# Optimization experiments

Hardware: AMD Instinct MI355X
Metric: run time of the kernel (lower is better)

The kernel has to match this reference:

```python
import jax, jax.numpy as jnp
import numpy as np

D_MODEL = 256
KSIZE = 16
EPS = 1e-5


def conv1d(x, w, b):
    # x: [B, C, N], w: [O, C, K], SAME padding over node axis
    y = jax.lax.conv_general_dilated(x, w, window_strides=(1,), padding='SAME',
                                     dimension_numbers=('NCH', 'OIH', 'NCH'))
    return y + b[None, :, None]


def layernorm(x, g, b):
    mu = jnp.mean(x, axis=-1, keepdims=True)
    var = jnp.mean(jnp.square(x - mu), axis=-1, keepdims=True)
    return (x - mu) * jax.lax.rsqrt(var + EPS) * g + b


def setup_inputs() -> dict:
    key = jax.random.key(0)
    ks = jax.random.split(key, 16)
    B, N, d, K = 4, 2048, D_MODEL, KSIZE
    conv_scale = 1.0 / np.sqrt(d * K)
    lin_scale = 1.0 / np.sqrt(d)
    return {
        'src': jax.random.normal(ks[0], (B, N, d), jnp.float32),
        'x_lst': jnp.zeros((B, N, N), jnp.float32),
        'adj': jax.random.randint(ks[1], (B, N, N), 0, 2, jnp.int32),
        'dis': jax.random.uniform(ks[2], (B, N, N), jnp.float32),
        'Wq': jax.random.normal(ks[3], (d, d, K), jnp.float32) * conv_scale,
        'bq': jnp.zeros((d,), jnp.float32),
        'Wk': jax.random.normal(ks[4], (d, d, K), jnp.float32) * conv_scale,
        'bk': jnp.zeros((d,), jnp.float32),
        'Wv': jax.random.normal(ks[5], (d, d, K), jnp.float32) * conv_scale,
        'bv': jnp.zeros((d,), jnp.float32),
        'W1': jax.random.normal(ks[6], (d, d), jnp.float32) * lin_scale,
        'b1': jnp.zeros((d,), jnp.float32),
        'W2': jax.random.normal(ks[7], (d, d), jnp.float32) * lin_scale,
        'b2': jnp.zeros((d,), jnp.float32),
        'W3': jax.random.normal(ks[8], (d, d), jnp.float32) * lin_scale,
        'b3': jnp.zeros((d,), jnp.float32),
        'g1': jnp.ones((d,), jnp.float32),
        'be1': jnp.zeros((d,), jnp.float32),
        'g2': jnp.ones((d,), jnp.float32),
        'be2': jnp.zeros((d,), jnp.float32),
    }


def reference(src, x_lst, adj, dis, Wq, bq, Wk, bk, Wv, bv,
              W1, b1, W2, b2, W3, b3, g1, be1, g2, be2):
    # ---- _ga_block: transpose to channel-major, graph attention ----
    x = jnp.swapaxes(src, -2, -1)                      # [B, d, N]
    q = conv1d(x, Wq, bq)                              # [B, d, N]
    k = conv1d(x, Wk, bk)
    v = conv1d(x, Wv, bv)
    scale = 1.0 / jnp.sqrt(jnp.asarray(D_MODEL, src.dtype))
    scores = jnp.einsum('bdn,bdm->bnm', q, k) * scale  # [B, N, N]
    scores = scores - dis                              # distance bias
    scores = jnp.where(adj > 0, scores, jnp.asarray(-1e9, scores.dtype))
    attn = jax.nn.softmax(scores, axis=-1)             # [B, N, N]
    x_lst_new = x_lst + attn                           # accumulated attention state
    out = jnp.einsum('bnm,bdm->bdn', attn, v)          # [B, d, N]
    x1 = jnp.swapaxes(out, -2, -1)                     # [B, N, d] (dropout = identity in eval)
    # ---- residual + norm1 ----
    h = layernorm(src + x1, g1, be1)
    # ---- 3-layer LeakyReLU MLP + residual + norm2 ----
    m = jax.nn.leaky_relu(h @ W1.T + b1)
    m = jax.nn.leaky_relu(m @ W2.T + b2)
    m = m @ W3.T + b3
    h = layernorm(h + m, g2, be2)
    return h, x_lst_new
```

## Files before the change

kernel.cpp:

```cpp
#include <hip/hip_runtime.h>
#include <stdint.h>

typedef _Float16 h16;
typedef _Float16 h4v __attribute__((ext_vector_type(4)));
typedef _Float16 h8v __attribute__((ext_vector_type(8)));
typedef float    f4v __attribute__((ext_vector_type(4)));
typedef int      i4v __attribute__((ext_vector_type(4)));

#define NBATCH 4
#define NNODE  2048
#define DM     256
#define NPAD   2063
#define QKELEM 2097152
#define PARTN  (8192 * 256)

__device__ __forceinline__ void async16(const void* g, void* l) {
#if __has_builtin(__builtin_amdgcn_global_load_lds)
  __builtin_amdgcn_global_load_lds((__attribute__((address_space(1))) void*)g,
                                   (__attribute__((address_space(3))) void*)l, 16, 0, 0);
#else
  *(f4v*)l = *(const f4v*)g;
#endif
}

#define BARRIER() do { asm volatile("" ::: "memory"); __builtin_amdgcn_s_barrier(); asm volatile("" ::: "memory"); } while (0)
#define MFMA16 __builtin_amdgcn_mfma_f32_16x16x32_f16

__device__ __forceinline__ void gemm_tile(
    const h16* Abase, int astride,
    const h16* Bbase, int bstride,
    h16* As, h16* Bs, f4v acc[4][4], int kiters)
{
  const int tid  = threadIdx.x;
  const int lane = tid & 63;
  const int wv   = tid >> 6;
  const int srow = tid >> 2;
  const int sch  = ((tid & 3) ^ ((tid >> 3) & 3)) * 8;
  const h16* gA0 = Abase + (long)srow * astride + sch;
  const h16* gA1 = Abase + (long)(srow + 64) * astride + sch;
  const h16* gB0 = Bbase + (long)srow * bstride + sch;
  const h16* gB1 = Bbase + (long)(srow + 64) * bstride + sch;
  h16* lA0 = As + tid * 8;
  h16* lA1 = As + 2048 + tid * 8;
  h16* lB0 = Bs + tid * 8;
  h16* lB1 = Bs + 2048 + tid * 8;
  const int swz = ((lane & 15) >> 1) & 3;
  const int qq  = ((lane >> 4) ^ swz) * 8;
  const int amr = ((wv & 1) * 64 + (lane & 15)) * 32 + qq;
  const int bnr = ((wv >> 1) * 64 + (lane & 15)) * 32 + qq;

  for (int kt = 0; kt < kiters; ++kt) {
    const int k0 = kt * 32;
    __syncthreads();
    async16(gA0 + k0, lA0);
    async16(gA1 + k0, lA1);
    async16(gB0 + k0, lB0);
    async16(gB1 + k0, lB1);
    asm volatile("s_waitcnt vmcnt(0)" ::: "memory");
    __syncthreads();
    h8v af[4], bf[4];
#pragma unroll
    for (int i = 0; i < 4; ++i) af[i] = *(const h8v*)(As + amr + i * 512);
#pragma unroll
    for (int j = 0; j < 4; ++j) bf[j] = *(const h8v*)(Bs + bnr + j * 512);
#pragma unroll
    for (int i = 0; i < 4; ++i)
#pragma unroll
      for (int j = 0; j < 4; ++j)
        acc[i][j] = MFMA16(af[i], bf[j], acc[i][j], 0, 0, 0);
  }
}

__device__ __forceinline__ void zero_acc(f4v acc[4][4]) {
#pragma unroll
  for (int i = 0; i < 4; ++i)
#pragma unroll
    for (int j = 0; j < 4; ++j) {
      f4v z = {0.f, 0.f, 0.f, 0.f};
      acc[i][j] = z;
    }
}

template<int ASTRIDE, int BSTRIDE>
__device__ __forceinline__ void gemm256_pipe(
    const h16* __restrict__ Abase, const h16* __restrict__ Bbase,
    h16* As, h16* Bs, f4v (&acc)[8][4], const int kiters)
{
  const int tid  = threadIdx.x;
  const int lane = tid & 63, wv = tid >> 6;

  const int rh = tid >> 3;
  const int cs = (((tid & 7) ^ ((tid >> 3) & 7)) << 3);
  const h16* AgT = Abase + (long)rh * ASTRIDE + cs;
  const h16* BgT = Bbase + (long)rh * BSTRIDE + cs;
  h16* lA = As + tid * 8;
  h16* lB = Bs + tid * 8;

  auto stageA = [&](int kt, int half) {
    h16* d = lA + ((kt & 1) << 14) + (half << 13);
    const h16* g = AgT + (long)half * 128 * ASTRIDE + kt * 64;
    async16(g, d);
    async16(g + 64 * ASTRIDE, d + 4096);
  };
  auto stageB = [&](int kt, int half) {
    h16* d = lB + ((kt & 1) << 14) + (half << 13);
    const h16* g = BgT + (long)half * 128 * BSTRIDE + kt * 64;
    async16(g, d);
    async16(g + 64 * BSTRIDE, d + 4096);
  };

  const int wr = wv >> 2, wc = wv & 3;
  const int e0 = (((lane >> 4) ^ (lane & 7)) << 3);
  const int e1 = e0 ^ 32;
  const h16* pA0 = As + (wr * 128 + (lane & 15)) * 64 + e0;
  const h16* pA1 = pA0 + (e1 - e0);
  const h16* pB0 = Bs + (wc * 64 + (lane & 15)) * 64 + e0;
  const h16* pB1 = pB0 + (e1 - e0);

#pragma unroll
  for (int i = 0; i < 8; ++i)
#pragma unroll
    for (int j = 0; j < 4; ++j) { f4v z = {0.f, 0.f, 0.f, 0.f}; acc[i][j] = z; }

  stageA(0, 0); stageA(0, 1); stageB(0, 0); stageB(0, 1); stageA(1, 0);
  asm volatile("s_waitcnt vmcnt(2)" ::: "memory");
  BARRIER();

#pragma unroll 1
  for (int kt = 0; kt < kiters; ++kt) {
    const int sb = (kt & 1) << 14;
    h8v ar[4][2], bL[2][2], bR[2][2];
#pragma unroll
    for (int i = 0; i < 4; ++i) {
      ar[i][0] = *(const h8v*)(pA0 + sb + i * 1024);
      ar[i][1] = *(const h8v*)(pA1 + sb + i * 1024);
    }
#pragma unroll
    for (int j = 0; j < 2; ++j) {
      bL[j][0] = *(const h8v*)(pB0 + sb + j * 1024);
      bL[j][1] = *(const h8v*)(pB1 + sb + j * 1024);
    }
    if (kt < kiters - 1) stageA(kt + 1, 1);
    BARRIER();
    __builtin_amdgcn_s_setprio(1);
#pragma unroll
    for (int i = 0; i < 4; ++i)
#pragma unroll
      for (int j = 0; j < 2; ++j) {
        acc[i][j] = MFMA16(ar[i][0], bL[j][0], acc[i][j], 0, 0, 0);
        acc[i][j] = MFMA16(ar[i][1], bL[j][1], acc[i][j], 0, 0, 0);
      }
    __builtin_amdgcn_s_setprio(0);
    BARRIER();
#pragma unroll
    for (int j = 0; j < 2; ++j) {
      bR[j][0] = *(const h8v*)(pB0 + sb + (j + 2) * 1024);
      bR[j][1] = *(const h8v*)(pB1 + sb + (j + 2) * 1024);
    }
    if (kt < kiters - 1) stageB(kt + 1, 0);
    BARRIER();
    __builtin_amdgcn_s_setprio(1);
#pragma unroll
    for (int i = 0; i < 4; ++i)
#pragma unroll
      for (int j = 0; j < 2; ++j) {
        acc[i][j + 2] = MFMA16(ar[i][0], bR[j][0], acc[i][j + 2], 0, 0, 0);
        acc[i][j + 2] = MFMA16(ar[i][1], bR[j][1], acc[i][j + 2], 0, 0, 0);
      }
    __builtin_amdgcn_s_setprio(0);
    BARRIER();
#pragma unroll
    for (int i = 0; i < 4; ++i) {
      ar[i][0] = *(const h8v*)(pA0 + sb + (i + 4) * 1024);
      ar[i][1] = *(const h8v*)(pA1 + sb + (i + 4) * 1024);
    }
    if (kt < kiters - 1) stageB(kt + 1, 1);
    BARRIER();
    __builtin_amdgcn_s_setprio(1);
#pragma unroll
    for (int i = 0; i < 4; ++i)
#pragma unroll
      for (int j = 0; j < 2; ++j) {
        acc[i + 4][j + 2] = MFMA16(ar[i][0], bR[j][0], acc[i + 4][j + 2], 0, 0, 0);
        acc[i + 4][j + 2] = MFMA16(ar[i][1], bR[j][1], acc[i + 4][j + 2], 0, 0, 0);
      }
    __builtin_amdgcn_s_setprio(0);
    BARRIER();
#pragma unroll
    for (int j = 0; j < 2; ++j) {
      bL[j][0] = *(const h8v*)(pB0 + sb + j * 1024);
      bL[j][1] = *(const h8v*)(pB1 + sb + j * 1024);
    }
    if (kt < kiters - 2) {
      stageA(kt + 2, 0);
      asm volatile("s_waitcnt vmcnt(2)" ::: "memory");
    } else if (kt == kiters - 2) {
      asm volatile("s_waitcnt vmcnt(0)" ::: "memory");
    }
    BARRIER();
    __builtin_amdgcn_s_setprio(1);
#pragma unroll
    for (int i = 0; i < 4; ++i)
#pragma unroll
      for (int j = 0; j < 2; ++j) {
        acc[i + 4][j] = MFMA16(ar[i][0], bL[j][0], acc[i + 4][j], 0, 0, 0);
        acc[i + 4][j] = MFMA16(ar[i][1], bL[j][1], acc[i + 4][j], 0, 0, 0);
      }
    __builtin_amdgcn_s_setprio(0);
    BARRIER();
  }
}

#define NSRC_BLK 8252
__global__ __launch_bounds__(256) void prep_all_kernel(
    const float* __restrict__ src,
    const float* __restrict__ Wq, const float* __restrict__ Wk, const float* __restrict__ Wv,
    const float* __restrict__ W1, const float* __restrict__ W2, const float* __restrict__ W3,
    h16* __restrict__ Xpad, h16* __restrict__ Wt, h16* __restrict__ Wl)
{
  __shared__ float plds[16][257];
  const int bi = blockIdx.x, tid = threadIdx.x;
  if (bi < NSRC_BLK) {
    int idx = bi * 256 + tid;
    int c = idx & 255;
    int row = idx >> 8;
    int b = row / NPAD;
    int n = row - b * NPAD;
    float v = 0.f;
    int ns = n - 7;
    if (ns >= 0 && ns < NNODE) v = src[((long)b * NNODE + ns) * DM + c];
    Xpad[idx] = (h16)v;
  } else if (bi < NSRC_BLK + 768) {
    const int q = bi - NSRC_BLK;
    const int w = q >> 8, o = q & 255;
    const float* W = (w == 0) ? Wq : (w == 1) ? Wk : Wv;
    const float* base = W + (long)o * 4096;
    f4v r0 = *(const f4v*)(base + tid * 16);
    f4v r1 = *(const f4v*)(base + tid * 16 + 4);
    f4v r2 = *(const f4v*)(base + tid * 16 + 8);
    f4v r3 = *(const f4v*)(base + tid * 16 + 12);
#pragma unroll
    for (int k = 0; k < 4; ++k) {
      plds[k][tid] = r0[k]; plds[4 + k][tid] = r1[k];
      plds[8 + k][tid] = r2[k]; plds[12 + k][tid] = r3[k];
    }
    __syncthreads();
    const int t = tid >> 4, c0 = (tid & 15) * 16;
    h16* out = Wt + ((long)(w * 256 + o)) * 4096 + t * 256 + c0;
    h8v o0, o1;
#pragma unroll
    for (int k = 0; k < 8; ++k) { o0[k] = (h16)plds[t][c0 + k]; o1[k] = (h16)plds[t][c0 + 8 + k]; }
    *(h8v*)out = o0;
    *(h8v*)(out + 8) = o1;
  } else {
    int idx = (bi - NSRC_BLK - 768) * 256 + tid;
    int w = idx >> 16;
    int rem = idx & 65535;
    const float* W = (w == 0) ? W1 : (w == 1) ? W2 : W3;
    Wl[idx] = (h16)W[rem];
  }
}

__global__ __launch_bounds__(512) void conv_gemm256_kernel(
    const h16* __restrict__ Xpad, const h16* __restrict__ Wt,
    h16* __restrict__ Qp, h16* __restrict__ Kp, h16* __restrict__ Vp)
{
  __shared__ __align__(16) h16 As[32768];
  __shared__ __align__(16) h16 Bs[32768];
  const int lane = threadIdx.x & 63, wv = threadIdx.x >> 6;
  const int mt = blockIdx.x, w = blockIdx.y, ks = blockIdx.z;
  const int m0 = mt * 256;
  const int b  = m0 >> 11, n0 = m0 & 2047;

  const h16* Abase = Xpad + ((long)(b * NPAD + n0) << 8) + ((long)ks << 11);
  const h16* Bbase = Wt + ((long)w << 20) + ((long)ks << 11);

  f4v acc[8][4];
  gemm256_pipe<256, 4096>(Abase, Bbase, As, Bs, acc, 32);

  h16* dst = ((w == 0) ? Qp : (w == 1) ? Kp : Vp) + (long)ks * QKELEM;
  const int wr = wv >> 2, wc = wv & 3;
  const int rb = (lane >> 4) * 4;
  const int cb = wc * 64 + (lane & 15);
  const int mrow0 = m0 + wr * 128;
#pragma unroll
  for (int i = 0; i < 8; ++i)
#pragma unroll
    for (int j = 0; j < 4; ++j) {
      const int gc = cb + j * 16;
#pragma unroll
      for (int e = 0; e < 4; ++e) {
        const int gr = mrow0 + i * 16 + rb + e;
        dst[(long)gr * 256 + gc] = (h16)acc[i][j][e];
      }
    }
}

__global__ __launch_bounds__(256) void conv_reduce_kernel(
    const h16* __restrict__ Qp, const h16* __restrict__ Kp, const h16* __restrict__ Vp,
    const float* __restrict__ bq, const float* __restrict__ bk, const float* __restrict__ bv,
    h16* __restrict__ Qb, h16* __restrict__ Kb, h16* __restrict__ Vt)
{
  __shared__ float T[64][65];
  const int bi = blockIdx.x, tid = threadIdx.x;
  if (bi < 2048) {
    const long gid = (long)bi * 256 + tid;
    const int which = gid >= (QKELEM / 8);
    const long e = (gid - (long)which * (QKELEM / 8)) * 8;
    const h16* P = which ? Kp : Qp;
    const float* bias = which ? bk : bq;
    h8v p0 = *(const h8v*)(P + e);
    h8v p1 = *(const h8v*)(P + QKELEM + e);
    const int c0 = (int)(e & 255);
    h8v o;
#pragma unroll
    for (int k = 0; k < 8; ++k) o[k] = (h16)((float)p0[k] + (float)p1[k] + bias[c0 + k]);
    *(h8v*)((which ? Kb : Qb) + e) = o;
  } else {
    const int q = bi - 2048;
    const int mt = q >> 2, ct = q & 3;
    const int m0 = mt * 64, c0 = ct * 64;
    const int b = m0 >> 11, n0 = m0 & 2047;
    const int rr = tid >> 3, cc = (tid & 7) * 8;
#pragma unroll
    for (int p = 0; p < 2; ++p) {
      const int r = p * 32 + rr;
      const long so = (long)(m0 + r) * 256 + c0 + cc;
      h8v p0 = *(const h8v*)(Vp + so);
      h8v p1 = *(const h8v*)(Vp + QKELEM + so);
#pragma unroll
      for (int e = 0; e < 8; ++e) T[r][cc + e] = (float)p0[e] + (float)p1[e];
    }
    __syncthreads();
#pragma unroll
    for (int p = 0; p < 2; ++p) {
      const int d = p * 32 + rr;
      const float bias_v = bv[c0 + d];
      h8v o;
#pragma unroll
      for (int e = 0; e < 8; ++e) o[e] = (h16)(T[cc + e][d] + bias_v);
      *(h8v*)(Vt + ((long)(b * 256 + c0 + d)) * 2048 + n0 + cc) = o;
    }
  }
}

__global__ __launch_bounds__(512) void scores_gemm256_kernel(
    const h16* __restrict__ Q, const h16* __restrict__ Km, h16* __restrict__ Sh)
{
  __shared__ __align__(16) h16 As[32768];
  __shared__ __align__(16) h16 Bs[32768];
  const int lane = threadIdx.x & 63, wv = threadIdx.x >> 6;
  const int nt = blockIdx.x, mt = blockIdx.y, b = blockIdx.z;

  const h16* Abase = Q + ((long)b * NNODE + nt * 256) * 256;
  const h16* Bbase = Km + ((long)b * NNODE + mt * 256) * 256;

  f4v acc[8][4];
  gemm256_pipe<256, 256>(Abase, Bbase, As, Bs, acc, 4);

  const int wr = wv >> 2, wc = wv & 3;
  const int rb = (lane >> 4) * 4;
  const int cb = wc * 64 + (lane & 15);
  h16* Srow = Sh + (long)b * NNODE * NNODE;
  const int row0 = nt * 256 + wr * 128;
  const int col0 = mt * 256;
#pragma unroll
  for (int i = 0; i < 8; ++i) {
#pragma unroll
    for (int e = 0; e < 4; ++e) {
      const long row = row0 + i * 16 + rb + e;
#pragma unroll
      for (int j = 0; j < 4; ++j) {
        const int col = col0 + cb + j * 16;
        Srow[row * 2048 + col] = (h16)(acc[i][j][e] * 0.0625f);
      }
    }
  }
}

__global__ __launch_bounds__(256) void softmax_kernel(
    h16* __restrict__ Sh, const float* __restrict__ dis, const int* __restrict__ adj,
    const float* __restrict__ x_lst, float* __restrict__ out_x)
{
  const int r = blockIdx.x;
  const long ro = (long)r * 2048;
  const int tid = threadIdx.x, lane = tid & 63, wv = tid >> 6;
  const int j0 = tid * 4;
  __shared__ float wmax[4], wsum[4];

  h4v sv0 = *(const h4v*)(Sh + ro + j0);
  h4v sv1 = *(const h4v*)(Sh + ro + 1024 + j0);
  f4v d0 = *(const f4v*)(dis + ro + j0);
  f4v d1 = *(const f4v*)(dis + ro + 1024 + j0);
  i4v a0 = *(const i4v*)(adj + ro + j0);
  i4v a1 = *(const i4v*)(adj + ro + 1024 + j0);

  float s[8];
#pragma unroll
  for (int k = 0; k < 4; ++k) s[k]     = (a0[k] > 0) ? ((float)sv0[k] - d0[k]) : -1e9f;
#pragma unroll
  for (int k = 0; k < 4; ++k) s[k + 4] = (a1[k] > 0) ? ((float)sv1[k] - d1[k]) : -1e9f;

  float m = s[0];
#pragma unroll
  for (int k = 1; k < 8; ++k) m = fmaxf(m, s[k]);
#pragma unroll
  for (int off = 32; off > 0; off >>= 1) m = fmaxf(m, __shfl_xor(m, off, 64));
  if (lane == 0) wmax[wv] = m;
  __syncthreads();
  m = fmaxf(fmaxf(wmax[0], wmax[1]), fmaxf(wmax[2], wmax[3]));

  float p[8], ls = 0.f;
#pragma unroll
  for (int k = 0; k < 8; ++k) { p[k] = __expf(s[k] - m); ls += p[k]; }
#pragma unroll
  for (int off = 32; off > 0; off >>= 1) ls += __shfl_xor(ls, off, 64);
  if (lane == 0) wsum[wv] = ls;
  __syncthreads();
  const float inv = 1.0f / (wsum[0] + wsum[1] + wsum[2] + wsum[3]);

  f4v x0 = *(const f4v*)(x_lst + ro + j0);
  f4v x1 = *(const f4v*)(x_lst + ro + 1024 + j0);
  f4v o0, o1;
  h4v pv0, pv1;
#pragma unroll
  for (int k = 0; k < 4; ++k) {
    const float a = p[k] * inv, bq = p[k + 4] * inv;
    o0[k] = x0[k] + a; o1[k] = x1[k] + bq;
    pv0[k] = (h16)a; pv1[k] = (h16)bq;
  }
  *(f4v*)(out_x + ro + j0) = o0;
  *(f4v*)(out_x + ro + 1024 + j0) = o1;
  *(h4v*)(Sh + ro + j0) = pv0;
  *(h4v*)(Sh + ro + 1024 + j0) = pv1;
}

__global__ __launch_bounds__(256) void av_gemm_kernel(
    const h16* __restrict__ Attn, const h16* __restrict__ Vt, h16* __restrict__ X1p)
{
  __shared__ __align__(16) h16 As[4096];
  __shared__ __align__(16) h16 Bs[4096];
  const int nt = blockIdx.x, b = blockIdx.z;
  const int ct = blockIdx.y & 1, ks = blockIdx.y >> 1;
  const h16* Abase = Attn + ((long)b * NNODE + nt * 128) * 2048 + ks * 1024;
  const h16* Bbase = Vt + ((long)b * 256 + ct * 128) * 2048 + ks * 1024;
  f4v acc[4][4];
  zero_acc(acc);
  gemm_tile(Abase, 2048, Bbase, 2048, As, Bs, acc, 32);

  const int lane = threadIdx.x & 63, wv = threadIdx.x >> 6;
  const int rbase = (wv & 1) * 64 + (lane >> 4) * 4;
  const int cbase = (wv >> 1) * 64 + (lane & 15);
  h16* dst = X1p + (long)ks * PARTN;
#pragma unroll
  for (int i = 0; i < 4; ++i) {
#pragma unroll
    for (int e = 0; e < 4; ++e) {
      const long row = (long)b * NNODE + nt * 128 + rbase + i * 16 + e;
#pragma unroll
      for (int j = 0; j < 4; ++j) {
        const int col = ct * 128 + cbase + j * 16;
        dst[row * 256 + col] = (h16)acc[i][j][e];
      }
    }
  }
}

__device__ __forceinline__ float wred_sum(float v) {
#pragma unroll
  for (int off = 32; off > 0; off >>= 1) v += __shfl_xor(v, off, 64);
  return v;
}

__global__ __launch_bounds__(256) void ln1_kernel(
    const float* __restrict__ X, const h16* __restrict__ Y, const h16* __restrict__ Y2,
    const float* __restrict__ g, const float* __restrict__ bb,
    float* __restrict__ outF, h16* __restrict__ outH)
{
  const int wv = threadIdx.x >> 6, lane = threadIdx.x & 63;
  const long r = (long)blockIdx.x * 4 + wv;
  const long off = r * 256 + lane * 4;
  f4v x = *(const f4v*)(X + off);
  h4v y = *(const h4v*)(Y + off);
  h4v y2 = *(const h4v*)(Y2 + off);
  float v[4];
  float sum = 0.f, sq = 0.f;
#pragma unroll
  for (int k = 0; k < 4; ++k) {
    v[k] = x[k] + (float)y[k] + (float)y2[k];
    sum += v[k]; sq += v[k] * v[k];
  }
  sum = wred_sum(sum);
  sq  = wred_sum(sq);
  const float mu = sum * (1.0f / 256.0f);
  const float var = sq * (1.0f / 256.0f) - mu * mu;
  const float rs = rsqrtf(var + 1e-5f);
  f4v gg = *(const f4v*)(g + lane * 4);
  f4v be = *(const f4v*)(bb + lane * 4);
  f4v o;
#pragma unroll
  for (int k = 0; k < 4; ++k) o[k] = (v[k] - mu) * rs * gg[k] + be[k];
  *(f4v*)(outF + off) = o;
  h4v hv;
#pragma unroll
  for (int k = 0; k < 4; ++k) hv[k] = (h16)o[k];
  *(h4v*)(outH + off) = hv;
}

__global__ __launch_bounds__(256) void mlp_fused_kernel(
    const h16* __restrict__ H16, const float* __restrict__ Hf,
    const h16* __restrict__ Wl,
    const float* __restrict__ b1, const float* __restrict__ b2, const float* __restrict__ b3,
    const float* __restrict__ g2, const float* __restrict__ be2,
    float* __restrict__ out_h)
{
  __shared__ h16 Xa[32][264];
  __shared__ h16 Xb[32][264];
  __shared__ __align__(16) h16 Bs[8192];
  const int tid = threadIdx.x, lane = tid & 63, wv = tid >> 6;
  const int m0 = blockIdx.x * 32;

  {
    const int r = tid >> 3, cq = (tid & 7) * 32;
    const h16* s = H16 + (long)(m0 + r) * 256 + cq;
#pragma unroll
    for (int k = 0; k < 4; ++k)
      *(h8v*)&Xa[r][cq + k * 8] = *(const h8v*)(s + k * 8);
  }

  const int srow = tid >> 2;
  const int sch  = ((tid & 3) ^ ((tid >> 3) & 3)) * 8;
  h16* lB = Bs + tid * 8;
  const int quad = lane >> 4;
  const float* biases[3] = {b1, b2, b3};

  for (int layer = 0; layer < 3; ++layer) {
    const h16* W = Wl + layer * 65536;
    const h16 (*Xi)[264] = (layer == 1) ? (const h16(*)[264])Xb : (const h16(*)[264])Xa;
    h16 (*Xo)[264] = (layer == 1) ? Xa : Xb;
    f4v acc[2][4];
#pragma unroll
    for (int i = 0; i < 2; ++i)
#pragma unroll
      for (int j = 0; j < 4; ++j) { f4v z = {0.f,0.f,0.f,0.f}; acc[i][j] = z; }

    for (int kt = 0; kt < 8; ++kt) {
      __syncthreads();
      const h16* gB = W + (long)srow * 256 + kt * 32 + sch;
      async16(gB, lB);
      async16(gB + 64 * 256, lB + 64 * 32);
      async16(gB + 128 * 256, lB + 128 * 32);
      async16(gB + 192 * 256, lB + 192 * 32);
      asm volatile("s_waitcnt vmcnt(0)" ::: "memory");
      __syncthreads();
      h8v af[2], bf[4];
#pragma unroll
      for (int i = 0; i < 2; ++i)
        af[i] = *(const h8v*)&Xi[i * 16 + (lane & 15)][kt * 32 + quad * 8];
#pragma unroll
      for (int j = 0; j < 4; ++j) {
        const int n = wv * 64 + j * 16 + (lane & 15);
        const int q = (quad ^ ((n >> 1) & 3)) * 8;
        bf[j] = *(const h8v*)(Bs + n * 32 + q);
      }
#pragma unroll
      for (int i = 0; i < 2; ++i)
#pragma unroll
        for (int j = 0; j < 4; ++j)
          acc[i][j] = MFMA16(af[i], bf[j], acc[i][j], 0, 0, 0);
    }
    const int rb = quad * 4;
    const int cb = wv * 64 + (lane & 15);
    const float* bias = biases[layer];
    const bool leaky = (layer < 2);
#pragma unroll
    for (int j = 0; j < 4; ++j) {
      const int col = cb + j * 16;
      const float bv = bias[col];
#pragma unroll
      for (int i = 0; i < 2; ++i)
#pragma unroll
        for (int e = 0; e < 4; ++e) {
          float v = acc[i][j][e] + bv;
          if (leaky) v = (v >= 0.f) ? v : 0.01f * v;
          Xo[i * 16 + rb + e][col] = (h16)v;
        }
    }
  }
  __syncthreads();

  const int r = tid >> 3, c0 = (tid & 7) * 32;
  const float* hrow = Hf + (long)(m0 + r) * 256 + c0;
  float v[32];
  float s = 0.f, sq = 0.f;
#pragma unroll
  for (int k8 = 0; k8 < 8; ++k8) {
    f4v h4 = *(const f4v*)(hrow + k8 * 4);
#pragma unroll
    for (int e = 0; e < 4; ++e) {
      float t = (float)Xb[r][c0 + k8 * 4 + e] + h4[e];
      v[k8 * 4 + e] = t; s += t; sq += t * t;
    }
  }
#pragma unroll
  for (int off = 1; off < 8; off <<= 1) { s += __shfl_xor(s, off, 64); sq += __shfl_xor(sq, off, 64); }
  const float mu = s * (1.0f / 256.0f);
  const float var = sq * (1.0f / 256.0f) - mu * mu;
  const float rs = rsqrtf(var + 1e-5f);
  float* orow = out_h + (long)(m0 + r) * 256 + c0;
#pragma unroll
  for (int k8 = 0; k8 < 8; ++k8) {
    f4v gg = *(const f4v*)(g2 + c0 + k8 * 4);
    f4v be = *(const f4v*)(be2 + c0 + k8 * 4);
    f4v o;
#pragma unroll
    for (int e = 0; e < 4; ++e) o[e] = (v[k8 * 4 + e] - mu) * rs * gg[e] + be[e];
    *(f4v*)(orow + k8 * 4) = o;
  }
}

extern "C" void kernel_launch(void* const* d_in, const int* in_sizes, int n_in,
                              void* d_out, int out_size, void* d_ws, size_t ws_size,
                              hipStream_t stream)
{
  const float* src  = (const float*)d_in[0];
  const float* xlst = (const float*)d_in[1];
  const int*   adj  = (const int*)d_in[2];
  const float* dis  = (const float*)d_in[3];
  const float* Wq   = (const float*)d_in[4];
  const float* bq   = (const float*)d_in[5];
  const float* Wk   = (const float*)d_in[6];
  const float* bk   = (const float*)d_in[7];
  const float* Wv   = (const float*)d_in[8];
  const float* bvp  = (const float*)d_in[9];
  const float* W1   = (const float*)d_in[10];
  const float* b1   = (const float*)d_in[11];
  const float* W2   = (const float*)d_in[12];
  const float* b2   = (const float*)d_in[13];
  const float* W3   = (const float*)d_in[14];
  const float* b3   = (const float*)d_in[15];
  const float* g1   = (const float*)d_in[16];
  const float* be1  = (const float*)d_in[17];
  const float* g2   = (const float*)d_in[18];
  const float* be2  = (const float*)d_in[19];
  (void)in_sizes; (void)n_in; (void)out_size; (void)ws_size;

  char* ws = (char*)d_ws;
  size_t off = 0;
  auto alloc = [&](size_t bytes) -> void* {
    void* p = ws + off;
    off += (bytes + 1023) & ~(size_t)1023;
    return p;
  };
  h16*   Xpad = (h16*)  alloc((size_t)NBATCH * NPAD * DM * 2);
  h16*   Wt   = (h16*)  alloc((size_t)3 * 256 * 4096 * 2);
  h16*   Wl   = (h16*)  alloc((size_t)3 * 256 * 256 * 2);
  h16*   Qb   = (h16*)  alloc((size_t)QKELEM * 2);
  h16*   Kb   = (h16*)  alloc((size_t)QKELEM * 2);
  h16*   Vt   = (h16*)  alloc((size_t)QKELEM * 2);
  char*  R    = (char*) alloc((size_t)66000 * 1024);
  h16*   Qp   = (h16*)R;
  h16*   Kp   = (h16*)(R + (size_t)2 * QKELEM * 2);
  h16*   Vp   = (h16*)(R + (size_t)4 * QKELEM * 2);
  h16*   Sh   = (h16*)R;
  h16*   X1p  = (h16*)(R + (size_t)8 * QKELEM * 2);
  float* H    = (float*)(R + (size_t)12 * QKELEM * 2);
  h16*   H16  = (h16*)((char*)H + (size_t)PARTN * 4);

  float* out_h = (float*)d_out;
  float* out_x = out_h + (size_t)NBATCH * NNODE * DM;

  prep_all_kernel<<<NSRC_BLK + 768 + 768, 256, 0, stream>>>(
      src, Wq, Wk, Wv, W1, W2, W3, Xpad, Wt, Wl);
  conv_gemm256_kernel<<<dim3(32, 3, 2), 512, 0, stream>>>(Xpad, Wt, Qp, Kp, Vp);
  conv_reduce_kernel<<<2048 + 512, 256, 0, stream>>>(
      Qp, Kp, Vp, bq, bk, bvp, Qb, Kb, Vt);
  scores_gemm256_kernel<<<dim3(8, 8, 4), 512, 0, stream>>>(Qb, Kb, Sh);
  softmax_kernel<<<NBATCH * NNODE, 256, 0, stream>>>(Sh, dis, adj, xlst, out_x);
  av_gemm_kernel<<<dim3(16, 4, 4), 256, 0, stream>>>(Sh, Vt, X1p);
  ln1_kernel<<<(NBATCH * NNODE) / 4, 256, 0, stream>>>(src, X1p, X1p + PARTN, g1, be1, H, H16);
  mlp_fused_kernel<<<NBATCH * NNODE / 32, 256, 0, stream>>>(
      H16, H, Wl, b1, b2, b3, g2, be2, out_h);
}
```

Measured before the change: 414.3 us.

## Fuse distance bias and adjacency mask into scores GEMM epilogue

Moves the dis subtraction and adj masking from the softmax kernel into the scores GEMM epilogue, so softmax only reads the fp16 scores. The scores GEMM also switches from 256x256 tiles with 512 threads to 128x128 tiles with 256 threads through the generic gemm_tile helper. The epilogue now does scalar, strided loads of dis and adj per element, which may coalesce poorly. Masked entries become -30000 in fp16 instead of -1e9, which gives the same softmax result unless an entire row is masked.

```diff
diff --git a/kernel.cpp b/kernel.cpp
--- a/kernel.cpp
+++ b/kernel.cpp
@@ -344,43 +344,44 @@
   }
 }
 
-__global__ __launch_bounds__(512) void scores_gemm256_kernel(
-    const h16* __restrict__ Q, const h16* __restrict__ Km, h16* __restrict__ Sh)
-{
-  __shared__ __align__(16) h16 As[32768];
-  __shared__ __align__(16) h16 Bs[32768];
+__global__ __launch_bounds__(256) void scores_gemm_kernel(
+    const h16* __restrict__ Q, const h16* __restrict__ Km,
+    const float* __restrict__ dis, const int* __restrict__ adj,
+    h16* __restrict__ Sh)
+{
+  __shared__ __align__(16) h16 As[4096];
+  __shared__ __align__(16) h16 Bs[4096];
+  const int nt = blockIdx.x, mt = blockIdx.y, b = blockIdx.z;
+  const h16* Abase = Q + ((long)b * NNODE + nt * 128) * 256;
+  const h16* Bbase = Km + ((long)b * NNODE + mt * 128) * 256;
+  f4v acc[4][4];
+  zero_acc(acc);
+  gemm_tile(Abase, 256, Bbase, 256, As, Bs, acc, 8);
+
   const int lane = threadIdx.x & 63, wv = threadIdx.x >> 6;
-  const int nt = blockIdx.x, mt = blockIdx.y, b = blockIdx.z;
-
-  const h16* Abase = Q + ((long)b * NNODE + nt * 256) * 256;
-  const h16* Bbase = Km + ((long)b * NNODE + mt * 256) * 256;
-
-  f4v acc[8][4];
-  gemm256_pipe<256, 256>(Abase, Bbase, As, Bs, acc, 4);
-
-  const int wr = wv >> 2, wc = wv & 3;
-  const int rb = (lane >> 4) * 4;
-  const int cb = wc * 64 + (lane & 15);
-  h16* Srow = Sh + (long)b * NNODE * NNODE;
-  const int row0 = nt * 256 + wr * 128;
-  const int col0 = mt * 256;
-#pragma unroll
-  for (int i = 0; i < 8; ++i) {
+  const int rbase = (wv & 1) * 64 + (lane >> 4) * 4;
+  const int cbase = (wv >> 1) * 64 + (lane & 15);
+  const long base = (long)b * NNODE * NNODE;
+#pragma unroll
+  for (int i = 0; i < 4; ++i) {
 #pragma unroll
     for (int e = 0; e < 4; ++e) {
-      const long row = row0 + i * 16 + rb + e;
+      const long row = nt * 128 + rbase + i * 16 + e;
+      const long ro = base + row * 2048 + mt * 128;
 #pragma unroll
       for (int j = 0; j < 4; ++j) {
-        const int col = col0 + cb + j * 16;
-        Srow[row * 2048 + col] = (h16)(acc[i][j][e] * 0.0625f);
+        const int col = cbase + j * 16;
+        const int a = adj[ro + col];
+        const float dd = dis[ro + col];
+        const float sv = acc[i][j][e] * 0.0625f - dd;
+        Sh[ro + col] = (a > 0) ? (h16)sv : (h16)(-30000.0f);
       }
     }
   }
 }
 
 __global__ __launch_bounds__(256) void softmax_kernel(
-    h16* __restrict__ Sh, const float* __restrict__ dis, const int* __restrict__ adj,
-    const float* __restrict__ x_lst, float* __restrict__ out_x)
+    h16* __restrict__ Sh, const float* __restrict__ x_lst, float* __restrict__ out_x)
 {
   const int r = blockIdx.x;
   const long ro = (long)r * 2048;
@@ -390,16 +391,10 @@
 
   h4v sv0 = *(const h4v*)(Sh + ro + j0);
   h4v sv1 = *(const h4v*)(Sh + ro + 1024 + j0);
-  f4v d0 = *(const f4v*)(dis + ro + j0);
-  f4v d1 = *(const f4v*)(dis + ro + 1024 + j0);
-  i4v a0 = *(const i4v*)(adj + ro + j0);
-  i4v a1 = *(const i4v*)(adj + ro + 1024 + j0);
 
   float s[8];
 #pragma unroll
-  for (int k = 0; k < 4; ++k) s[k]     = (a0[k] > 0) ? ((float)sv0[k] - d0[k]) : -1e9f;
-#pragma unroll
-  for (int k = 0; k < 4; ++k) s[k + 4] = (a1[k] > 0) ? ((float)sv1[k] - d1[k]) : -1e9f;
+  for (int k = 0; k < 4; ++k) { s[k] = (float)sv0[k]; s[k + 4] = (float)sv1[k]; }
 
   float m = s[0];
 #pragma unroll
@@ -675,8 +670,8 @@
   conv_gemm256_kernel<<<dim3(32, 3, 2), 512, 0, stream>>>(Xpad, Wt, Qp, Kp, Vp);
   conv_reduce_kernel<<<2048 + 512, 256, 0, stream>>>(
       Qp, Kp, Vp, bq, bk, bvp, Qb, Kb, Vt);
-  scores_gemm256_kernel<<<dim3(8, 8, 4), 512, 0, stream>>>(Qb, Kb, Sh);
-  softmax_kernel<<<NBATCH * NNODE, 256, 0, stream>>>(Sh, dis, adj, xlst, out_x);
+  scores_gemm_kernel<<<dim3(16, 16, 4), 256, 0, stream>>>(Qb, Kb, dis, adj, Sh);
+  softmax_kernel<<<NBATCH * NNODE, 256, 0, stream>>>(Sh, xlst, out_x);
   av_gemm_kernel<<<dim3(16, 4, 4), 256, 0, stream>>>(Sh, Vt, X1p);
   ln1_kernel<<<(NBATCH * NNODE) / 4, 256, 0, stream>>>(src, X1p, X1p + PARTN, g1, be1, H, H16);
   mlp_fused_kernel<<<NBATCH * NNODE / 32, 256, 0, stream>>>(
```

New measurement: 421.4 us. No clear change (+1.7%).
